# Optimization experiments

Hardware: AMD Instinct MI355X
Metric: run time of the kernel (lower is better)

## Reference

```python
import jax, jax.numpy as jnp
import numpy as np


def setup_inputs() -> dict:
    key = jax.random.key(0)
    k1, k2, k3, k4 = jax.random.split(key, 4)
    B, S, E = 8, 4096, 1024
    H, D = 256, 4  # num_heads, n_wires_per_head; H*D == E
    scale = 1.0 / np.sqrt(E)
    return {
        "x": jax.random.normal(k1, (B, S, E), dtype=jnp.float32),
        "W_proj": jax.random.normal(k2, (E, E), dtype=jnp.float32) * scale,
        "W_combine": jax.random.normal(k3, (E, E), dtype=jnp.float32) * scale,
        "phi": jax.random.normal(k4, (H, D), dtype=jnp.float32),
    }


def reference(x, W_proj, W_combine, phi):
    # Linear projection (no bias): torch Linear computes x @ W.T
    proj = jnp.einsum("bse,fe->bsf", x, W_proj)  # [B,S,E]
    B, S, E = proj.shape
    H, D = phi.shape
    # Quantum head per token: RX-encode each feature, trainable RX, PauliZ measure.
    # RX(a)RX(b) = RX(a+b); <0|RX(t)^dag Z RX(t)|0> = cos(t)  =>  cos(x + phi)
    qout = jnp.cos(proj.reshape(B, S, H, D) + phi)  # broadcast phi[h,d]
    qout = qout.reshape(B, S, E)
    return jnp.einsum("bse,fe->bsf", qout, W_combine)
```

## Files before the change

kernel.cpp:

```cpp
#include <hip/hip_runtime.h>
#include <cstdint>
#include <cstddef>


typedef __attribute__((ext_vector_type(8))) short short8;
typedef __attribute__((ext_vector_type(4))) float f32x4;

__device__ __forceinline__ unsigned short f2bf(float f) {
  unsigned u = __float_as_uint(f);
  u += 0x7FFFu + ((u >> 16) & 1u);
  return (unsigned short)(u >> 16);
}

__device__ __forceinline__ void async_load16(const void* g, const void* l) {
  __builtin_amdgcn_global_load_lds(
      (const __attribute__((address_space(1))) void*)g,
      (__attribute__((address_space(3))) void*)l,
      16, 0, 0);
}

__global__ __launch_bounds__(256) void cast_f32_bf16(
    const float* __restrict__ src, unsigned short* __restrict__ dst, int n) {
  int i = (blockIdx.x * 256 + threadIdx.x) * 4;
  if (i >= n) return;
  const float4 v = *(const float4*)(src + i);
  ushort4 o;
  o.x = f2bf(v.x);
  o.y = f2bf(v.y);
  o.z = f2bf(v.z);
  o.w = f2bf(v.w);
  *(ushort4*)(dst + i) = o;
}

constexpr int TM = 128, TN = 128, BK = 32;
constexpr int Kdim = 1024, Ndim = 1024;

template <int EPI>
__global__ __launch_bounds__(256, 2) void gemm_bt(
    const unsigned short* __restrict__ A,
    const unsigned short* __restrict__ B,
    const float* __restrict__ phi,
    void* __restrict__ Cout) {
  __shared__ unsigned short As[TM * BK];
  __shared__ unsigned short Bs[TN * BK];

  const int tid  = threadIdx.x;
  const int lane = tid & 63;
  const int wv   = tid >> 6;
  const int m_blk = blockIdx.x >> 3;
  const int n_blk = blockIdx.x & 7;
  const long row0 = (long)m_blk * TM;
  const int  col0 = n_blk * TN;

  const int s_row  = lane >> 2;
  const int s_colb = (lane & 3) * 16;

  const int lane15 = lane & 15;
  const int quad   = lane >> 4;
  const int wm = (wv >> 1) * 64;
  const int wn = (wv & 1) * 64;

  f32x4 acc[4][4];
#pragma unroll
  for (int mi = 0; mi < 4; ++mi)
#pragma unroll
    for (int ni = 0; ni < 4; ++ni) {
      f32x4 z = {0.f, 0.f, 0.f, 0.f};
      acc[mi][ni] = z;
    }

  for (int k0 = 0; k0 < Kdim; k0 += BK) {
#pragma unroll
    for (int j = 0; j < 2; ++j) {
      const int chunk = wv * 2 + j;
      const int row = chunk * 16 + s_row;
      const char* ga = (const char*)(A + (row0 + row) * Kdim + k0) + s_colb;
      async_load16(ga, (const char*)As + chunk * 1024);
      const char* gb = (const char*)(B + (long)(col0 + row) * Kdim + k0) + s_colb;
      async_load16(gb, (const char*)Bs + chunk * 1024);
    }
    __syncthreads();

    short8 af[4], bfr[4];
#pragma unroll
    for (int mi = 0; mi < 4; ++mi)
      af[mi] = *(const short8*)(As + (wm + mi * 16 + lane15) * BK + quad * 8);
#pragma unroll
    for (int ni = 0; ni < 4; ++ni)
      bfr[ni] = *(const short8*)(Bs + (wn + ni * 16 + lane15) * BK + quad * 8);
#pragma unroll
    for (int mi = 0; mi < 4; ++mi)
#pragma unroll
      for (int ni = 0; ni < 4; ++ni)
        acc[mi][ni] = __builtin_amdgcn_mfma_f32_16x16x32_bf16(
            af[mi], bfr[ni], acc[mi][ni], 0, 0, 0);
    __syncthreads();
  }

  if (EPI == 1) {
    unsigned short* Q = (unsigned short*)Cout;
    float ph[4];
#pragma unroll
    for (int ni = 0; ni < 4; ++ni)
      ph[ni] = phi[col0 + wn + ni * 16 + lane15];
#pragma unroll
    for (int mi = 0; mi < 4; ++mi) {
      const long rbase = row0 + wm + mi * 16 + quad * 4;
#pragma unroll
      for (int ni = 0; ni < 4; ++ni) {
        const int c = col0 + wn + ni * 16 + lane15;
#pragma unroll
        for (int r = 0; r < 4; ++r) {
          float v = __cosf(acc[mi][ni][r] + ph[ni]);
          Q[(rbase + r) * Ndim + c] = f2bf(v);
        }
      }
    }
  } else {
    float* C = (float*)Cout;
#pragma unroll
    for (int mi = 0; mi < 4; ++mi) {
      const long rbase = row0 + wm + mi * 16 + quad * 4;
#pragma unroll
      for (int ni = 0; ni < 4; ++ni) {
        const int c = col0 + wn + ni * 16 + lane15;
#pragma unroll
        for (int r = 0; r < 4; ++r)
          C[(rbase + r) * Ndim + c] = acc[mi][ni][r];
      }
    }
  }
}

extern "C" void kernel_launch(void* const* d_in, const int* in_sizes, int n_in,
                              void* d_out, int out_size, void* d_ws, size_t ws_size,
                              hipStream_t stream) {
  const float* x   = (const float*)d_in[0];
  const float* Wp  = (const float*)d_in[1];
  const float* Wc  = (const float*)d_in[2];
  const float* phi = (const float*)d_in[3];
  float* out = (float*)d_out;

  char* ws = (char*)d_ws;
  unsigned short* Abf  = (unsigned short*)(ws);
  unsigned short* Qbf  = (unsigned short*)(ws + (size_t)67108864);
  unsigned short* Wpbf = (unsigned short*)(ws + (size_t)134217728);
  unsigned short* Wcbf = (unsigned short*)(ws + (size_t)136314880);

  cast_f32_bf16<<<32768, 256, 0, stream>>>(x, Abf, 33554432);
  cast_f32_bf16<<<1024, 256, 0, stream>>>(Wp, Wpbf, 1048576);
  cast_f32_bf16<<<1024, 256, 0, stream>>>(Wc, Wcbf, 1048576);

  gemm_bt<1><<<2048, 256, 0, stream>>>(Abf, Wpbf, phi, (void*)Qbf);
  gemm_bt<0><<<2048, 256, 0, stream>>>(Qbf, Wcbf, nullptr, (void*)out);

  (void)in_sizes; (void)n_in; (void)out_size; (void)ws_size;
}
```

Measured before the change: 413.9 us.

## Fuse fp32-to-bf16 activation cast into first GEMM A-tile loading with register prefetch

Removes the standalone cast kernel over x and the bf16 copy it wrote. The first GEMM now reads fp32 x directly, converts to bf16 in registers with a simpler round-half-up pack, and writes to LDS. The next K-slice is prefetched into registers while the MFMAs run. The two weight casts are merged into one launch. The trade-off is that the first GEMM reads twice the A bytes from global memory, A loads are synchronous instead of async-to-LDS, and register pressure rises.

Result: slower. 436.3 us (+5.4%).

```diff
diff --git a/kernel.cpp b/kernel.cpp
--- a/kernel.cpp
+++ b/kernel.cpp
@@ -10,6 +10,11 @@
   unsigned u = __float_as_uint(f);
   u += 0x7FFFu + ((u >> 16) & 1u);
   return (unsigned short)(u >> 16);
+}
+
+__device__ __forceinline__ unsigned pack2bf(float lo, float hi) {
+  return ((__float_as_uint(lo) + 0x8000u) >> 16) |
+         ((__float_as_uint(hi) + 0x8000u) & 0xFFFF0000u);
 }
 
 __device__ __forceinline__ void async_load16(const void* g, const void* l) {
@@ -19,28 +24,29 @@
       16, 0, 0);
 }
 
-__global__ __launch_bounds__(256) void cast_f32_bf16(
-    const float* __restrict__ src, unsigned short* __restrict__ dst, int n) {
+__global__ __launch_bounds__(256) void cast_w(
+    const float* __restrict__ Wp, const float* __restrict__ Wc,
+    unsigned short* __restrict__ dp, unsigned short* __restrict__ dc) {
   int i = (blockIdx.x * 256 + threadIdx.x) * 4;
-  if (i >= n) return;
-  const float4 v = *(const float4*)(src + i);
+  const float* s;
+  unsigned short* d;
+  int j;
+  if (i < 1048576) { s = Wp; d = dp; j = i; }
+  else             { s = Wc; d = dc; j = i - 1048576; }
+  const float4 v = *(const float4*)(s + j);
   ushort4 o;
-  o.x = f2bf(v.x);
-  o.y = f2bf(v.y);
-  o.z = f2bf(v.z);
-  o.w = f2bf(v.w);
-  *(ushort4*)(dst + i) = o;
+  o.x = f2bf(v.x); o.y = f2bf(v.y); o.z = f2bf(v.z); o.w = f2bf(v.w);
+  *(ushort4*)(d + j) = o;
 }
 
 constexpr int TM = 128, TN = 128, BK = 32;
 constexpr int Kdim = 1024, Ndim = 1024;
 
-template <int EPI>
-__global__ __launch_bounds__(256, 2) void gemm_bt(
-    const unsigned short* __restrict__ A,
+__global__ __launch_bounds__(256, 2) void gemm1_fused(
+    const float* __restrict__ X,
     const unsigned short* __restrict__ B,
     const float* __restrict__ phi,
-    void* __restrict__ Cout) {
+    unsigned short* __restrict__ Q) {
   __shared__ unsigned short As[TM * BK];
   __shared__ unsigned short Bs[TN * BK];
 
@@ -52,6 +58,104 @@
   const long row0 = (long)m_blk * TM;
   const int  col0 = n_blk * TN;
 
+  const int rowA  = tid >> 1;
+  const int halfA = tid & 1;
+  const float* gA = X + (row0 + rowA) * Kdim + halfA * 16;
+  unsigned* wA = (unsigned*)(As + rowA * BK + halfA * 16);
+
+  const int s_row  = lane >> 2;
+  const int s_colb = (lane & 3) * 16;
+
+  const int lane15 = lane & 15;
+  const int quad   = lane >> 4;
+  const int wm = (wv >> 1) * 64;
+  const int wn = (wv & 1) * 64;
+
+  f32x4 acc[4][4];
+#pragma unroll
+  for (int mi = 0; mi < 4; ++mi)
+#pragma unroll
+    for (int ni = 0; ni < 4; ++ni) {
+      f32x4 z = {0.f, 0.f, 0.f, 0.f};
+      acc[mi][ni] = z;
+    }
+
+  float4 a0, a1, a2, a3;
+  {
+    const float4* p = (const float4*)(gA);
+    a0 = p[0]; a1 = p[1]; a2 = p[2]; a3 = p[3];
+  }
+
+  for (int k0 = 0; k0 < Kdim; k0 += BK) {
+    wA[0] = pack2bf(a0.x, a0.y); wA[1] = pack2bf(a0.z, a0.w);
+    wA[2] = pack2bf(a1.x, a1.y); wA[3] = pack2bf(a1.z, a1.w);
+    wA[4] = pack2bf(a2.x, a2.y); wA[5] = pack2bf(a2.z, a2.w);
+    wA[6] = pack2bf(a3.x, a3.y); wA[7] = pack2bf(a3.z, a3.w);
+#pragma unroll
+    for (int j = 0; j < 2; ++j) {
+      const int chunk = wv * 2 + j;
+      const int row = chunk * 16 + s_row;
+      const char* gb = (const char*)(B + (long)(col0 + row) * Kdim + k0) + s_colb;
+      async_load16(gb, (const char*)Bs + chunk * 1024);
+    }
+    __syncthreads();
+
+    {
+      const int kn = (k0 + BK) & (Kdim - 1);
+      const float4* p = (const float4*)(gA + kn);
+      a0 = p[0]; a1 = p[1]; a2 = p[2]; a3 = p[3];
+    }
+
+    short8 af[4], bfr[4];
+#pragma unroll
+    for (int mi = 0; mi < 4; ++mi)
+      af[mi] = *(const short8*)(As + (wm + mi * 16 + lane15) * BK + quad * 8);
+#pragma unroll
+    for (int ni = 0; ni < 4; ++ni)
+      bfr[ni] = *(const short8*)(Bs + (wn + ni * 16 + lane15) * BK + quad * 8);
+#pragma unroll
+    for (int mi = 0; mi < 4; ++mi)
+#pragma unroll
+      for (int ni = 0; ni < 4; ++ni)
+        acc[mi][ni] = __builtin_amdgcn_mfma_f32_16x16x32_bf16(
+            af[mi], bfr[ni], acc[mi][ni], 0, 0, 0);
+    __syncthreads();
+  }
+
+  float ph[4];
+#pragma unroll
+  for (int ni = 0; ni < 4; ++ni)
+    ph[ni] = phi[col0 + wn + ni * 16 + lane15];
+#pragma unroll
+  for (int mi = 0; mi < 4; ++mi) {
+    const long rbase = row0 + wm + mi * 16 + quad * 4;
+#pragma unroll
+    for (int ni = 0; ni < 4; ++ni) {
+      const int c = col0 + wn + ni * 16 + lane15;
+#pragma unroll
+      for (int r = 0; r < 4; ++r) {
+        float v = __cosf(acc[mi][ni][r] + ph[ni]);
+        Q[(rbase + r) * Ndim + c] = f2bf(v);
+      }
+    }
+  }
+}
+
+__global__ __launch_bounds__(256, 2) void gemm2_bt(
+    const unsigned short* __restrict__ A,
+    const unsigned short* __restrict__ B,
+    float* __restrict__ C) {
+  __shared__ unsigned short As[TM * BK];
+  __shared__ unsigned short Bs[TN * BK];
+
+  const int tid  = threadIdx.x;
+  const int lane = tid & 63;
+  const int wv   = tid >> 6;
+  const int m_blk = blockIdx.x >> 3;
+  const int n_blk = blockIdx.x & 7;
+  const long row0 = (long)m_blk * TM;
+  const int  col0 = n_blk * TN;
+
   const int s_row  = lane >> 2;
   const int s_colb = (lane & 3) * 16;
 
@@ -97,37 +201,15 @@
     __syncthreads();
   }
 
-  if (EPI == 1) {
-    unsigned short* Q = (unsigned short*)Cout;
-    float ph[4];
-#pragma unroll
-    for (int ni = 0; ni < 4; ++ni)
-      ph[ni] = phi[col0 + wn + ni * 16 + lane15];
-#pragma unroll
-    for (int mi = 0; mi < 4; ++mi) {
-      const long rbase = row0 + wm + mi * 16 + quad * 4;
-#pragma unroll
-      for (int ni = 0; ni < 4; ++ni) {
-        const int c = col0 + wn + ni * 16 + lane15;
-#pragma unroll
-        for (int r = 0; r < 4; ++r) {
-          float v = __cosf(acc[mi][ni][r] + ph[ni]);
-          Q[(rbase + r) * Ndim + c] = f2bf(v);
-        }
-      }
-    }
-  } else {
-    float* C = (float*)Cout;
-#pragma unroll
-    for (int mi = 0; mi < 4; ++mi) {
-      const long rbase = row0 + wm + mi * 16 + quad * 4;
-#pragma unroll
-      for (int ni = 0; ni < 4; ++ni) {
-        const int c = col0 + wn + ni * 16 + lane15;
-#pragma unroll
-        for (int r = 0; r < 4; ++r)
-          C[(rbase + r) * Ndim + c] = acc[mi][ni][r];
-      }
+#pragma unroll
+  for (int mi = 0; mi < 4; ++mi) {
+    const long rbase = row0 + wm + mi * 16 + quad * 4;
+#pragma unroll
+    for (int ni = 0; ni < 4; ++ni) {
+      const int c = col0 + wn + ni * 16 + lane15;
+#pragma unroll
+      for (int r = 0; r < 4; ++r)
+        C[(rbase + r) * Ndim + c] = acc[mi][ni][r];
     }
   }
 }
@@ -142,17 +224,13 @@
   float* out = (float*)d_out;
 
   char* ws = (char*)d_ws;
-  unsigned short* Abf  = (unsigned short*)(ws);
-  unsigned short* Qbf  = (unsigned short*)(ws + (size_t)67108864);
-  unsigned short* Wpbf = (unsigned short*)(ws + (size_t)134217728);
-  unsigned short* Wcbf = (unsigned short*)(ws + (size_t)136314880);
-
-  cast_f32_bf16<<<32768, 256, 0, stream>>>(x, Abf, 33554432);
-  cast_f32_bf16<<<1024, 256, 0, stream>>>(Wp, Wpbf, 1048576);
-  cast_f32_bf16<<<1024, 256, 0, stream>>>(Wc, Wcbf, 1048576);
-
-  gemm_bt<1><<<2048, 256, 0, stream>>>(Abf, Wpbf, phi, (void*)Qbf);
-  gemm_bt<0><<<2048, 256, 0, stream>>>(Qbf, Wcbf, nullptr, (void*)out);
+  unsigned short* Qbf  = (unsigned short*)(ws);
+  unsigned short* Wpbf = (unsigned short*)(ws + (size_t)67108864);
+  unsigned short* Wcbf = (unsigned short*)(ws + (size_t)69206016);
+
+  cast_w<<<2048, 256, 0, stream>>>(Wp, Wc, Wpbf, Wcbf);
+  gemm1_fused<<<2048, 256, 0, stream>>>(x, Wpbf, phi, Qbf);
+  gemm2_bt<<<2048, 256, 0, stream>>>(Qbf, Wcbf, out);
 
   (void)in_sizes; (void)n_in; (void)out_size; (void)ws_size;
 }
```
